# Kernel optimization log

Measured on AMD Instinct MI355X. Metric: run time of the kernel, lower is better.

The kernel has to match this reference:

```python
import jax, jax.numpy as jnp
import numpy as np

DIM = 256
HEADS = 8
HEAD_DIM = 32
WS = 64
MLP = 1024
INNER = HEADS * HEAD_DIM
EPS = 1e-5


def setup_inputs() -> dict:
    key = jax.random.key(0)
    ks = jax.random.split(key, 10)
    B, N = 2, 65536
    s = lambda fan_in: 1.0 / np.sqrt(fan_in)
    return {
        "x": jax.random.normal(ks[0], (B, N, DIM), jnp.float32),
        "w_qkv": jax.random.normal(ks[1], (DIM, 3 * INNER), jnp.float32) * s(DIM),
        "w_out": jax.random.normal(ks[2], (INNER, DIM), jnp.float32) * s(INNER),
        "b_out": jnp.zeros((DIM,), jnp.float32),
        "pos_emb": jax.random.normal(ks[3], (WS, WS), jnp.float32),
        "ln1_g": jnp.ones((DIM,), jnp.float32),
        "ln1_b": jnp.zeros((DIM,), jnp.float32),
        "w1": jax.random.normal(ks[4], (DIM, MLP), jnp.float32) * s(DIM),
        "b1": jnp.zeros((MLP,), jnp.float32),
        "w2": jax.random.normal(ks[5], (MLP, DIM), jnp.float32) * s(MLP),
        "b2": jnp.zeros((DIM,), jnp.float32),
        "ln2_g": jnp.ones((DIM,), jnp.float32),
        "ln2_b": jnp.zeros((DIM,), jnp.float32),
    }


def layernorm(x, g, b):
    mu = jnp.mean(x, axis=-1, keepdims=True)
    var = jnp.var(x, axis=-1, keepdims=True)
    return (x - mu) * jax.lax.rsqrt(var + EPS) * g + b


def window_attn(x, w_qkv, w_out, b_out, pos_emb):
    # shifted window attention (displacement = WS // 2)
    disp = WS // 2
    x = jnp.roll(x, -disp, axis=1)
    b, n, _ = x.shape
    n_w = n // WS
    qkv = x @ w_qkv  # [b, n, 3*inner]
    qkv = qkv.reshape(b, n_w, WS, 3, HEADS, HEAD_DIM)
    q = jnp.transpose(qkv[:, :, :, 0], (0, 3, 1, 2, 4))  # [b, h, n_w, ws, d]
    k = jnp.transpose(qkv[:, :, :, 1], (0, 3, 1, 2, 4))
    v = jnp.transpose(qkv[:, :, :, 2], (0, 3, 1, 2, 4))
    scale = HEAD_DIM ** -0.5
    dots = jnp.einsum("bhwid,bhwjd->bhwij", q, k) * scale + pos_emb
    attn = jax.nn.softmax(dots, axis=-1)
    out = jnp.einsum("bhwij,bhwjd->bhwid", attn, v)
    out = jnp.transpose(out, (0, 2, 3, 1, 4)).reshape(b, n, INNER)
    out = out @ w_out + b_out
    return jnp.roll(out, disp, axis=1)


def reference(x, w_qkv, w_out, b_out, pos_emb, ln1_g, ln1_b, w1, b1, w2, b2, ln2_g, ln2_b):
    # PointSwinBlock: Residual(PreNorm(attn)) then Residual(PreNorm(ffn))
    x = x + window_attn(layernorm(x, ln1_g, ln1_b), w_qkv, w_out, b_out, pos_emb)
    h = layernorm(x, ln2_g, ln2_b)
    h = jax.nn.gelu(h @ w1 + b1, approximate=False) @ w2 + b2
    return x + h
```

## Files before the change

### kernel.cpp

```cpp
#include <hip/hip_runtime.h>
#include <hip/hip_bf16.h>
#include <math.h>
#include <stdint.h>

#define DIM   256
#define NSEQ  65536
#define NTOK  131072
#define HEADS 8
#define HD    32
#define WSZ   64
#define NWIN  2048
#define QKVN  768
#define MLPD  1024
#define LNEPS 1e-5f

typedef __bf16 bf16;
typedef __bf16 bf16x8 __attribute__((ext_vector_type(8)));
typedef __bf16 bf16x4 __attribute__((ext_vector_type(4)));
typedef float  f32x4  __attribute__((ext_vector_type(4)));

__device__ __forceinline__ int roll_row(int r) {
  return (r & 0x10000) | ((r + 32) & 0xFFFF);
}

__device__ __forceinline__ float fast_gelu(float v) {
  const float x2 = v * v;
  const float z2 = v * __builtin_fmaf(x2, 0.07135481630268f, 1.5957691216057308f);
  const float e  = __expf(z2);
  const float r  = __builtin_amdgcn_rcpf(e + 1.0f);
  return __builtin_fmaf(-v, r, v);
}

template<int NY>
__device__ __forceinline__ void grid_swz(int& mBase, int& nBase) {
  const int nwg  = gridDim.x;
  const int lin  = blockIdx.x;
  const int orig = (lin & 7) * (nwg >> 3) + (lin >> 3);
  mBase = (orig / NY) * 128;
  nBase = (orig % NY) * 128;
}

__device__ __forceinline__ void stage16(const bf16* g, bf16* l) {
#if __has_builtin(__builtin_amdgcn_global_load_lds)
  __builtin_amdgcn_global_load_lds((const __attribute__((address_space(1))) void*)g,
                                   (__attribute__((address_space(3))) void*)l, 16, 0, 0);
#else
  int lane = threadIdx.x & 63;
  *(uint4*)((char*)l + lane * 16) = *(const uint4*)g;
#endif
}

template<int K, int LDB, bool ROLL>
__device__ __forceinline__ void gemm_tile(const bf16* __restrict__ A,
                                          const bf16* __restrict__ Bt,
                                          int mBase, int nBase,
                                          bf16* sA, bf16* sB,
                                          f32x4 acc[4][4])
{
  const int tid  = threadIdx.x;
  const int wave = tid >> 6;
  const int lane = tid & 63;
  const int slot = lane & 3;
  const int swz  = (lane >> 3) & 3;
  const int rloc = lane >> 2;
  const int chunk = ((slot ^ swz) * 8);

  int lr0 = mBase + wave * 32 + rloc;
  int lr1 = lr0 + 16;
  int ar0 = ROLL ? roll_row(lr0) : lr0;
  int ar1 = ROLL ? roll_row(lr1) : lr1;
  const bf16* gA0 = A + (size_t)ar0 * K + chunk;
  const bf16* gA1 = A + (size_t)ar1 * K + chunk;
  const bf16* gB0 = Bt + (size_t)(nBase + wave * 32 + rloc) * LDB + chunk;
  const bf16* gB1 = Bt + (size_t)(nBase + wave * 32 + rloc + 16) * LDB + chunk;

  bf16* dA0 = sA + (wave * 32 +  0) * 32;
  bf16* dA1 = sA + (wave * 32 + 16) * 32;
  bf16* dB0 = sB + (wave * 32 +  0) * 32;
  bf16* dB1 = sB + (wave * 32 + 16) * 32;

  const int m0 = (wave & 1) * 64;
  const int n0 = (wave >> 1) * 64;
  const int c    = lane & 15;
  const int quad = lane >> 4;

  int fa[4], fb[4];
#pragma unroll
  for (int t = 0; t < 4; ++t) {
    int rowA = m0 + t * 16 + c;
    fa[t] = rowA * 32 + ((quad ^ ((rowA >> 1) & 3)) * 8);
    int rowB = n0 + t * 16 + c;
    fb[t] = rowB * 32 + ((quad ^ ((rowB >> 1) & 3)) * 8);
  }

  const f32x4 fzero = {0.f, 0.f, 0.f, 0.f};
#pragma unroll
  for (int i = 0; i < 4; ++i)
#pragma unroll
    for (int j = 0; j < 4; ++j) acc[i][j] = fzero;

  stage16(gA0, dA0);
  stage16(gA1, dA1);
  stage16(gB0, dB0);
  stage16(gB1, dB1);
  __syncthreads();

  int cur = 0;
  for (int k0 = 0; k0 < K; k0 += 32) {
    const int nxt = cur ^ 1;
    if (k0 + 32 < K) {
      const int o = nxt * 4096;
      stage16(gA0 + k0 + 32, dA0 + o);
      stage16(gA1 + k0 + 32, dA1 + o);
      stage16(gB0 + k0 + 32, dB0 + o);
      stage16(gB1 + k0 + 32, dB1 + o);
    }
    const int co = cur * 4096;
    bf16x8 afr[4], bfr[4];
#pragma unroll
    for (int t = 0; t < 4; ++t) {
      afr[t] = *(const bf16x8*)(sA + co + fa[t]);
      bfr[t] = *(const bf16x8*)(sB + co + fb[t]);
    }
#pragma unroll
    for (int i = 0; i < 4; ++i)
#pragma unroll
      for (int j = 0; j < 4; ++j)
        acc[i][j] = __builtin_amdgcn_mfma_f32_16x16x32_bf16(afr[i], bfr[j], acc[i][j], 0, 0, 0);
    __syncthreads();
    cur = nxt;
  }
}

__global__ __launch_bounds__(256) void k_prep(const float* __restrict__ wqkv,
                                              const float* __restrict__ wout,
                                              const float* __restrict__ w1,
                                              const float* __restrict__ w2,
                                              const float* __restrict__ pos,
                                              bf16* __restrict__ wqkvT, bf16* __restrict__ woutT,
                                              bf16* __restrict__ w1T, bf16* __restrict__ w2T,
                                              float* __restrict__ posP)
{
  const int total = 768 * 256 + 256 * 256 + 1024 * 256 + 256 * 1024 + 4096;
  for (int i = blockIdx.x * 256 + threadIdx.x; i < total; i += gridDim.x * 256) {
    int j = i;
    if (j < 768 * 256) { int n = j >> 8, k = j & 255; wqkvT[j] = (bf16)wqkv[k * 768 + n]; continue; }
    j -= 768 * 256;
    if (j < 256 * 256) { int n = j >> 8, k = j & 255; woutT[j] = (bf16)wout[k * 256 + n]; continue; }
    j -= 256 * 256;
    if (j < 1024 * 256) { int n = j >> 8, k = j & 255; w1T[j] = (bf16)w1[k * 1024 + n]; continue; }
    j -= 1024 * 256;
    if (j < 256 * 1024) { int n = j >> 10, k = j & 1023; w2T[j] = (bf16)w2[k * 256 + n]; continue; }
    j -= 256 * 1024;
    {
      int lane = j & 63, t = j >> 6;
      int nt = t & 3, r = (t >> 2) & 3, mt = t >> 4;
      int ii = mt * 16 + (lane >> 4) * 4 + r, jj = nt * 16 + (lane & 15);
      posP[j] = pos[ii * 64 + jj];
    }
  }
}

__global__ __launch_bounds__(256) void k_ln(const float* __restrict__ x,
                                            const float* __restrict__ gam,
                                            const float* __restrict__ bet,
                                            bf16* __restrict__ out)
{
  const int wave = threadIdx.x >> 6, lane = threadIdx.x & 63;
  const int token = blockIdx.x * 4 + wave;
  const float4 v = ((const float4*)x)[(size_t)token * 64 + lane];
  float s = v.x + v.y + v.z + v.w;
  float q = v.x * v.x + v.y * v.y + v.z * v.z + v.w * v.w;
#pragma unroll
  for (int off = 32; off; off >>= 1) { s += __shfl_xor(s, off); q += __shfl_xor(q, off); }
  const float mu = s * (1.f / 256.f);
  const float var = q * (1.f / 256.f) - mu * mu;
  const float rs = rsqrtf(var + LNEPS);
  const float4 gv = ((const float4*)gam)[lane];
  const float4 bv = ((const float4*)bet)[lane];
  bf16x4 o;
  o[0] = (bf16)((v.x - mu) * rs * gv.x + bv.x);
  o[1] = (bf16)((v.y - mu) * rs * gv.y + bv.y);
  o[2] = (bf16)((v.z - mu) * rs * gv.z + bv.z);
  o[3] = (bf16)((v.w - mu) * rs * gv.w + bv.w);
  *(bf16x4*)(out + (size_t)token * 256 + lane * 4) = o;
}

__global__ __launch_bounds__(256, 2) void k_gemm_qkv(const bf16* __restrict__ h1,
                                                     const bf16* __restrict__ wqkvT,
                                                     bf16* __restrict__ qkv)
{
  __shared__ __align__(16) bf16 sA[2 * 128 * 32];
  __shared__ __align__(16) bf16 sB[2 * 128 * 32];
  f32x4 acc[4][4];
  int mBase, nBase;
  grid_swz<6>(mBase, nBase);
  gemm_tile<256, 256, true>(h1, wqkvT, mBase, nBase, sA, sB, acc);
  const int lane = threadIdx.x & 63, wave = threadIdx.x >> 6;
  const int c = lane & 15, quad = lane >> 4;
  const int rowBase = mBase + (wave & 1) * 64 + quad * 4;
  const int colBase = nBase + (wave >> 1) * 64 + c;
#pragma unroll
  for (int i = 0; i < 4; ++i)
#pragma unroll
    for (int j = 0; j < 4; ++j)
#pragma unroll
      for (int r = 0; r < 4; ++r)
        qkv[(size_t)(rowBase + i * 16 + r) * QKVN + (colBase + j * 16)] = (bf16)acc[i][j][r];
}

__global__ __launch_bounds__(256, 2) void k_attn(const bf16* __restrict__ qkv,
                                                 const float* __restrict__ posP,
                                                 bf16* __restrict__ attn)
{
  __shared__ __align__(16) bf16 sQ[4][64 * 40];
  __shared__ __align__(16) bf16 sK[4][64 * 40];
  __shared__ __align__(16) bf16 sV[4][32 * 72];
  const int tid = threadIdx.x;
  const int wave = tid >> 6, lane = tid & 63;
  const int gh = blockIdx.y * 4 + wave;
  const int win = blockIdx.x;
  const int c = lane & 15, quad = lane >> 4;
  const size_t base = (size_t)win * 64 * QKVN;

  {
    const int row = lane >> 2;
    const int col = (lane & 3) * 8;
#pragma unroll
    for (int i = 0; i < 4; ++i) {
      int rr = i * 16 + row;
      *(uint4*)(&sQ[wave][rr * 40 + col]) = *(const uint4*)(qkv + base + (size_t)rr * QKVN + gh * 32 + col);
      *(uint4*)(&sK[wave][rr * 40 + col]) = *(const uint4*)(qkv + base + (size_t)rr * QKVN + 256 + gh * 32 + col);
    }
  }
  {
    const int d = lane & 31, jh = lane >> 5;
#pragma unroll
    for (int it = 0; it < 32; ++it) {
      int j = it * 2 + jh;
      sV[wave][d * 72 + j] = qkv[base + (size_t)j * QKVN + 512 + gh * 32 + d];
    }
  }

  const f32x4 fzero = {0.f, 0.f, 0.f, 0.f};
  f32x4 sacc[4][4];
#pragma unroll
  for (int i = 0; i < 4; ++i)
#pragma unroll
    for (int j = 0; j < 4; ++j) sacc[i][j] = fzero;
  bf16x8 qf[4], kf[4];
#pragma unroll
  for (int t = 0; t < 4; ++t) {
    qf[t] = *(const bf16x8*)(&sQ[wave][(t * 16 + c) * 40 + quad * 8]);
    kf[t] = *(const bf16x8*)(&sK[wave][(t * 16 + c) * 40 + quad * 8]);
  }
#pragma unroll
  for (int i = 0; i < 4; ++i)
#pragma unroll
    for (int j = 0; j < 4; ++j)
      sacc[i][j] = __builtin_amdgcn_mfma_f32_16x16x32_bf16(qf[i], kf[j], sacc[i][j], 0, 0, 0);

  const float scale = 0.17677669529663687f;
  float p[4][4][4];
#pragma unroll
  for (int i = 0; i < 4; ++i)
#pragma unroll
    for (int j = 0; j < 4; ++j)
#pragma unroll
      for (int r = 0; r < 4; ++r)
        p[i][j][r] = sacc[i][j][r] * scale + posP[(((i * 4 + r) * 4 + j) << 6) + lane];

  float mx[4][4], rcp[4][4];
#pragma unroll
  for (int i = 0; i < 4; ++i)
#pragma unroll
    for (int r = 0; r < 4; ++r) {
      float m = fmaxf(fmaxf(p[i][0][r], p[i][1][r]), fmaxf(p[i][2][r], p[i][3][r]));
      m = fmaxf(m, __shfl_xor(m, 1)); m = fmaxf(m, __shfl_xor(m, 2));
      m = fmaxf(m, __shfl_xor(m, 4)); m = fmaxf(m, __shfl_xor(m, 8));
      mx[i][r] = m;
    }
#pragma unroll
  for (int i = 0; i < 4; ++i)
#pragma unroll
    for (int r = 0; r < 4; ++r) {
#pragma unroll
      for (int j = 0; j < 4; ++j) p[i][j][r] = __expf(p[i][j][r] - mx[i][r]);
      float t = p[i][0][r] + p[i][1][r] + p[i][2][r] + p[i][3][r];
      t += __shfl_xor(t, 1); t += __shfl_xor(t, 2); t += __shfl_xor(t, 4); t += __shfl_xor(t, 8);
      rcp[i][r] = 1.0f / t;
    }
#pragma unroll
  for (int i = 0; i < 4; ++i)
#pragma unroll
    for (int j = 0; j < 4; ++j)
#pragma unroll
      for (int r = 0; r < 4; ++r) p[i][j][r] *= rcp[i][r];

  f32x4 oacc[4][2];
#pragma unroll
  for (int i = 0; i < 4; ++i) { oacc[i][0] = fzero; oacc[i][1] = fzero; }
#pragma unroll
  for (int half = 0; half < 2; ++half) {
#pragma unroll
    for (int i = 0; i < 4; ++i)
#pragma unroll
      for (int j2 = 0; j2 < 2; ++j2)
#pragma unroll
        for (int r = 0; r < 4; ++r)
          sQ[wave][(i * 16 + quad * 4 + r) * 40 + j2 * 16 + c] = (bf16)p[i][half * 2 + j2][r];
    bf16x8 pf[4], vf[2];
#pragma unroll
    for (int t = 0; t < 4; ++t)
      pf[t] = *(const bf16x8*)(&sQ[wave][(t * 16 + c) * 40 + quad * 8]);
#pragma unroll
    for (int n2 = 0; n2 < 2; ++n2)
      vf[n2] = *(const bf16x8*)(&sV[wave][(n2 * 16 + c) * 72 + half * 32 + quad * 8]);
#pragma unroll
    for (int i = 0; i < 4; ++i)
#pragma unroll
      for (int n2 = 0; n2 < 2; ++n2)
        oacc[i][n2] = __builtin_amdgcn_mfma_f32_16x16x32_bf16(pf[i], vf[n2], oacc[i][n2], 0, 0, 0);
  }

#pragma unroll
  for (int i = 0; i < 4; ++i)
#pragma unroll
    for (int n2 = 0; n2 < 2; ++n2)
#pragma unroll
      for (int r = 0; r < 4; ++r)
        attn[(size_t)(win * 64 + i * 16 + quad * 4 + r) * DIM + gh * 32 + n2 * 16 + c] = (bf16)oacc[i][n2][r];
}

__global__ __launch_bounds__(256, 2) void k_gemm_proj(const bf16* __restrict__ attn,
                                                      const bf16* __restrict__ woutT,
                                                      const float* __restrict__ x,
                                                      const float* __restrict__ b_out,
                                                      float* __restrict__ x2)
{
  __shared__ __align__(16) bf16 sA[2 * 128 * 32];
  __shared__ __align__(16) bf16 sB[2 * 128 * 32];
  f32x4 acc[4][4];
  int mBase, nBase;
  grid_swz<2>(mBase, nBase);
  gemm_tile<256, 256, false>(attn, woutT, mBase, nBase, sA, sB, acc);
  const int lane = threadIdx.x & 63, wave = threadIdx.x >> 6;
  const int c = lane & 15, quad = lane >> 4;
  const int rowBase = mBase + (wave & 1) * 64 + quad * 4;
  const int colBase = nBase + (wave >> 1) * 64 + c;
#pragma unroll
  for (int i = 0; i < 4; ++i)
#pragma unroll
    for (int r = 0; r < 4; ++r) {
      const int rp = rowBase + i * 16 + r;
      const size_t rowoff = (size_t)roll_row(rp) * DIM;
#pragma unroll
      for (int j = 0; j < 4; ++j) {
        const int col = colBase + j * 16;
        x2[rowoff + col] = acc[i][j][r] + b_out[col] + x[rowoff + col];
      }
    }
}

template<int LDC, int NY>
__global__ __launch_bounds__(256, 2) void k_gemm_mlp1(const bf16* __restrict__ h2,
                                                      const bf16* __restrict__ w1Th,
                                                      const float* __restrict__ b1h,
                                                      bf16* __restrict__ g)
{
  __shared__ __align__(16) bf16 sA[2 * 128 * 32];
  __shared__ __align__(16) bf16 sB[2 * 128 * 32];
  f32x4 acc[4][4];
  int mBase, nBase;
  grid_swz<NY>(mBase, nBase);
  gemm_tile<256, 256, false>(h2, w1Th, mBase, nBase, sA, sB, acc);
  const int lane = threadIdx.x & 63, wave = threadIdx.x >> 6;
  const int c = lane & 15, quad = lane >> 4;
  const int rowBase = mBase + (wave & 1) * 64 + quad * 4;
  const int colBase = nBase + (wave >> 1) * 64 + c;
#pragma unroll
  for (int i = 0; i < 4; ++i)
#pragma unroll
    for (int j = 0; j < 4; ++j) {
      const int col = colBase + j * 16;
      const float bb = b1h[col];
#pragma unroll
      for (int r = 0; r < 4; ++r) {
        const float v = acc[i][j][r] + bb;
        g[(size_t)(rowBase + i * 16 + r) * LDC + col] = (bf16)fast_gelu(v);
      }
    }
}

template<int K>
__global__ __launch_bounds__(256, 2) void k_gemm_mlp2(const bf16* __restrict__ g,
                                                      const bf16* __restrict__ w2Th,
                                                      const float* __restrict__ b2,
                                                      float* __restrict__ out,
                                                      int first)
{
  __shared__ __align__(16) bf16 sA[2 * 128 * 32];
  __shared__ __align__(16) bf16 sB[2 * 128 * 32];
  f32x4 acc[4][4];
  int mBase, nBase;
  grid_swz<2>(mBase, nBase);
  gemm_tile<K, 1024, false>(g, w2Th, mBase, nBase, sA, sB, acc);
  const int lane = threadIdx.x & 63, wave = threadIdx.x >> 6;
  const int c = lane & 15, quad = lane >> 4;
  const int rowBase = mBase + (wave & 1) * 64 + quad * 4;
  const int colBase = nBase + (wave >> 1) * 64 + c;
#pragma unroll
  for (int i = 0; i < 4; ++i)
#pragma unroll
    for (int j = 0; j < 4; ++j) {
      const int col = colBase + j * 16;
      const float bb = first ? b2[col] : 0.0f;
#pragma unroll
      for (int r = 0; r < 4; ++r) {
        const size_t off = (size_t)(rowBase + i * 16 + r) * DIM + col;
        out[off] = out[off] + acc[i][j][r] + bb;
      }
    }
}

extern "C" void kernel_launch(void* const* d_in, const int* in_sizes, int n_in,
                              void* d_out, int out_size, void* d_ws, size_t ws_size,
                              hipStream_t stream) {
  const float* x    = (const float*)d_in[0];
  const float* wqkv = (const float*)d_in[1];
  const float* wout = (const float*)d_in[2];
  const float* bo   = (const float*)d_in[3];
  const float* pos  = (const float*)d_in[4];
  const float* l1g  = (const float*)d_in[5];
  const float* l1b  = (const float*)d_in[6];
  const float* w1   = (const float*)d_in[7];
  const float* b1   = (const float*)d_in[8];
  const float* w2   = (const float*)d_in[9];
  const float* b2   = (const float*)d_in[10];
  const float* l2g  = (const float*)d_in[11];
  const float* l2b  = (const float*)d_in[12];
  float* out = (float*)d_out;

  char* ws = (char*)d_ws;
  const size_t WEIGHTS_SZ = (size_t)768 * 256 * 2 + 256 * 256 * 2 + 1024 * 256 * 2
                          + 256 * 1024 * 2 + 4096 * 4;
  const size_t FUSED_NEED = 67108864ull + 268435456ull + WEIGHTS_SZ;
  const bool fused = ws_size >= FUSED_NEED;

  bf16* h1   = (bf16*)ws;
  bf16* qkv  = (bf16*)(ws + 67108864);
  bf16* attn = h1;
  bf16* h2;
  bf16* gbuf;
  char* wp;
  if (fused) {
    h2   = (bf16*)ws;
    gbuf = (bf16*)(ws + 67108864);
    wp   = ws + 67108864 + 268435456;
  } else {
    h2   = qkv;
    gbuf = (bf16*)(ws + 134217728);
    wp   = ws + 268435456;
  }
  bf16* wqkvT = (bf16*)wp;  wp += 768 * 256 * 2;
  bf16* woutT = (bf16*)wp;  wp += 256 * 256 * 2;
  bf16* w1T   = (bf16*)wp;  wp += 1024 * 256 * 2;
  bf16* w2T   = (bf16*)wp;  wp += 256 * 1024 * 2;
  float* posP = (float*)wp;

  k_prep<<<dim3(1024), dim3(256), 0, stream>>>(wqkv, wout, w1, w2, pos, wqkvT, woutT, w1T, w2T, posP);
  k_ln<<<dim3(NTOK / 4), dim3(256), 0, stream>>>(x, l1g, l1b, h1);
  k_gemm_qkv<<<dim3(6144), dim3(256), 0, stream>>>(h1, wqkvT, qkv);
  k_attn<<<dim3(NWIN, 2), dim3(256), 0, stream>>>(qkv, posP, attn);
  k_gemm_proj<<<dim3(2048), dim3(256), 0, stream>>>(attn, woutT, x, bo, out);
  k_ln<<<dim3(NTOK / 4), dim3(256), 0, stream>>>(out, l2g, l2b, h2);
  if (fused) {
    k_gemm_mlp1<1024, 8><<<dim3(8192), dim3(256), 0, stream>>>(h2, w1T, b1, gbuf);
    k_gemm_mlp2<1024><<<dim3(2048), dim3(256), 0, stream>>>(gbuf, w2T, b2, out, 1);
  } else {
    for (int half = 0; half < 2; ++half) {
      k_gemm_mlp1<512, 4><<<dim3(4096), dim3(256), 0, stream>>>(h2, w1T + half * 512 * 256, b1 + half * 512, gbuf);
      k_gemm_mlp2<512><<<dim3(2048), dim3(256), 0, stream>>>(gbuf, w2T + half * 512, b2, out, half == 0 ? 1 : 0);
    }
  }
}
```

Baseline: 797.5 us.

## Stage full-K A tile in LDS and read B fragments directly from global

Replaces the double-buffered 32-wide K-step GEMM with a loop that loads a whole 128x256 A tile into LDS in one XOR-swizzled phase, then runs eight K-steps with no barriers between them. B (weight) fragments are now loaded straight from global memory/L2 into registers instead of through LDS. This cuts the number of barriers and LDS staging of weights, but removes the overlap between loading and computing within a phase. It also raises LDS use to 64KB per block, which may limit occupancy to one or two blocks per CU.

```diff
diff --git a/kernel.cpp b/kernel.cpp
--- a/kernel.cpp
+++ b/kernel.cpp
@@ -51,84 +51,68 @@
 }
 
 template<int K, int LDB, bool ROLL>
-__device__ __forceinline__ void gemm_tile(const bf16* __restrict__ A,
+__device__ __forceinline__ void gemm_bigA(const bf16* __restrict__ A,
                                           const bf16* __restrict__ Bt,
                                           int mBase, int nBase,
-                                          bf16* sA, bf16* sB,
+                                          bf16* sA,
                                           f32x4 acc[4][4])
 {
   const int tid  = threadIdx.x;
   const int wave = tid >> 6;
   const int lane = tid & 63;
-  const int slot = lane & 3;
-  const int swz  = (lane >> 3) & 3;
-  const int rloc = lane >> 2;
-  const int chunk = ((slot ^ swz) * 8);
-
-  int lr0 = mBase + wave * 32 + rloc;
-  int lr1 = lr0 + 16;
-  int ar0 = ROLL ? roll_row(lr0) : lr0;
-  int ar1 = ROLL ? roll_row(lr1) : lr1;
-  const bf16* gA0 = A + (size_t)ar0 * K + chunk;
-  const bf16* gA1 = A + (size_t)ar1 * K + chunk;
-  const bf16* gB0 = Bt + (size_t)(nBase + wave * 32 + rloc) * LDB + chunk;
-  const bf16* gB1 = Bt + (size_t)(nBase + wave * 32 + rloc + 16) * LDB + chunk;
-
-  bf16* dA0 = sA + (wave * 32 +  0) * 32;
-  bf16* dA1 = sA + (wave * 32 + 16) * 32;
-  bf16* dB0 = sB + (wave * 32 +  0) * 32;
-  bf16* dB1 = sB + (wave * 32 + 16) * 32;
-
+  const int c    = lane & 15;
+  const int quad = lane >> 4;
   const int m0 = (wave & 1) * 64;
   const int n0 = (wave >> 1) * 64;
-  const int c    = lane & 15;
-  const int quad = lane >> 4;
-
-  int fa[4], fb[4];
+
+  const f32x4 fzero = {0.f, 0.f, 0.f, 0.f};
+#pragma unroll
+  for (int i = 0; i < 4; ++i)
+#pragma unroll
+    for (int j = 0; j < 4; ++j) acc[i][j] = fzero;
+
+  const int w5    = tid >> 5;
+  const int cphys = tid & 31;
+
+  int fa[4], r31[4];
 #pragma unroll
   for (int t = 0; t < 4; ++t) {
-    int rowA = m0 + t * 16 + c;
-    fa[t] = rowA * 32 + ((quad ^ ((rowA >> 1) & 3)) * 8);
-    int rowB = n0 + t * 16 + c;
-    fb[t] = rowB * 32 + ((quad ^ ((rowB >> 1) & 3)) * 8);
-  }
-
-  const f32x4 fzero = {0.f, 0.f, 0.f, 0.f};
-#pragma unroll
-  for (int i = 0; i < 4; ++i)
-#pragma unroll
-    for (int j = 0; j < 4; ++j) acc[i][j] = fzero;
-
-  stage16(gA0, dA0);
-  stage16(gA1, dA1);
-  stage16(gB0, dB0);
-  stage16(gB1, dB1);
-  __syncthreads();
-
-  int cur = 0;
-  for (int k0 = 0; k0 < K; k0 += 32) {
-    const int nxt = cur ^ 1;
-    if (k0 + 32 < K) {
-      const int o = nxt * 4096;
-      stage16(gA0 + k0 + 32, dA0 + o);
-      stage16(gA1 + k0 + 32, dA1 + o);
-      stage16(gB0 + k0 + 32, dB0 + o);
-      stage16(gB1 + k0 + 32, dB1 + o);
-    }
-    const int co = cur * 4096;
-    bf16x8 afr[4], bfr[4];
-#pragma unroll
-    for (int t = 0; t < 4; ++t) {
-      afr[t] = *(const bf16x8*)(sA + co + fa[t]);
-      bfr[t] = *(const bf16x8*)(sB + co + fb[t]);
-    }
-#pragma unroll
-    for (int i = 0; i < 4; ++i)
+    const int r = m0 + t * 16 + c;
+    fa[t]  = r * 256;
+    r31[t] = r & 31;
+  }
+
+  const bf16* bp = Bt + (size_t)(nBase + n0 + c) * LDB + quad * 8;
+
+  constexpr int NPH = K / 256;
+  for (int ph = 0; ph < NPH; ++ph) {
+    if (ph) __syncthreads();
+    const int k0 = ph * 256;
+#pragma unroll
+    for (int s = 0; s < 16; ++s) {
+      const int row  = s * 8 + w5;
+      const int csrc = cphys ^ (row & 31);
+      const int ar   = ROLL ? roll_row(mBase + row) : (mBase + row);
+      stage16(A + (size_t)ar * K + k0 + csrc * 8,
+              sA + (size_t)(s * 256 + wave * 64) * 8);
+    }
+    __syncthreads();
+#pragma unroll
+    for (int ks = 0; ks < 8; ++ks) {
+      bf16x8 b[4];
 #pragma unroll
       for (int j = 0; j < 4; ++j)
-        acc[i][j] = __builtin_amdgcn_mfma_f32_16x16x32_bf16(afr[i], bfr[j], acc[i][j], 0, 0, 0);
-    __syncthreads();
-    cur = nxt;
+        b[j] = *(const bf16x8*)(bp + (size_t)(j * 16) * LDB + k0 + ks * 32);
+      bf16x8 a[4];
+#pragma unroll
+      for (int t = 0; t < 4; ++t)
+        a[t] = *(const bf16x8*)(sA + fa[t] + (((ks * 4 + quad) ^ r31[t]) << 3));
+#pragma unroll
+      for (int i = 0; i < 4; ++i)
+#pragma unroll
+        for (int j = 0; j < 4; ++j)
+          acc[i][j] = __builtin_amdgcn_mfma_f32_16x16x32_bf16(a[i], b[j], acc[i][j], 0, 0, 0);
+    }
   }
 }
 
@@ -190,12 +174,11 @@
                                                      const bf16* __restrict__ wqkvT,
                                                      bf16* __restrict__ qkv)
 {
-  __shared__ __align__(16) bf16 sA[2 * 128 * 32];
-  __shared__ __align__(16) bf16 sB[2 * 128 * 32];
+  __shared__ __align__(16) bf16 sA[128 * 256];
   f32x4 acc[4][4];
   int mBase, nBase;
   grid_swz<6>(mBase, nBase);
-  gemm_tile<256, 256, true>(h1, wqkvT, mBase, nBase, sA, sB, acc);
+  gemm_bigA<256, 256, true>(h1, wqkvT, mBase, nBase, sA, acc);
   const int lane = threadIdx.x & 63, wave = threadIdx.x >> 6;
   const int c = lane & 15, quad = lane >> 4;
   const int rowBase = mBase + (wave & 1) * 64 + quad * 4;
@@ -338,12 +321,11 @@
                                                       const float* __restrict__ b_out,
                                                       float* __restrict__ x2)
 {
-  __shared__ __align__(16) bf16 sA[2 * 128 * 32];
-  __shared__ __align__(16) bf16 sB[2 * 128 * 32];
+  __shared__ __align__(16) bf16 sA[128 * 256];
   f32x4 acc[4][4];
   int mBase, nBase;
   grid_swz<2>(mBase, nBase);
-  gemm_tile<256, 256, false>(attn, woutT, mBase, nBase, sA, sB, acc);
+  gemm_bigA<256, 256, false>(attn, woutT, mBase, nBase, sA, acc);
   const int lane = threadIdx.x & 63, wave = threadIdx.x >> 6;
   const int c = lane & 15, quad = lane >> 4;
   const int rowBase = mBase + (wave & 1) * 64 + quad * 4;
@@ -368,12 +350,11 @@
                                                       const float* __restrict__ b1h,
                                                       bf16* __restrict__ g)
 {
-  __shared__ __align__(16) bf16 sA[2 * 128 * 32];
-  __shared__ __align__(16) bf16 sB[2 * 128 * 32];
+  __shared__ __align__(16) bf16 sA[128 * 256];
   f32x4 acc[4][4];
   int mBase, nBase;
   grid_swz<NY>(mBase, nBase);
-  gemm_tile<256, 256, false>(h2, w1Th, mBase, nBase, sA, sB, acc);
+  gemm_bigA<256, 256, false>(h2, w1Th, mBase, nBase, sA, acc);
   const int lane = threadIdx.x & 63, wave = threadIdx.x >> 6;
   const int c = lane & 15, quad = lane >> 4;
   const int rowBase = mBase + (wave & 1) * 64 + quad * 4;
@@ -399,12 +380,11 @@
                                                       float* __restrict__ out,
                                                       int first)
 {
-  __shared__ __align__(16) bf16 sA[2 * 128 * 32];
-  __shared__ __align__(16) bf16 sB[2 * 128 * 32];
+  __shared__ __align__(16) bf16 sA[128 * 256];
   f32x4 acc[4][4];
   int mBase, nBase;
   grid_swz<2>(mBase, nBase);
-  gemm_tile<K, 1024, false>(g, w2Th, mBase, nBase, sA, sB, acc);
+  gemm_bigA<K, 1024, false>(g, w2Th, mBase, nBase, sA, acc);
   const int lane = threadIdx.x & 63, wave = threadIdx.x >> 6;
   const int c = lane & 15, quad = lane >> 4;
   const int rowBase = mBase + (wave & 1) * 64 + quad * 4;
```

Measured after the change: 948.6 us. 1.19x slower.
